# Performance work log

Measured on AMD Instinct MI355X. Metric: run time of the kernel, lower is better.

The kernel has to match this reference:

```python
import jax, jax.numpy as jnp
import numpy as np

NUM_BUCKETS = 32
MAX_DISTANCE = 128
NEG = -1000000.0


def t5_position_bucket(seq_len):
    # distances from the single query (at position seq_len-1) to keys 0..seq_len-1
    n = (seq_len - 1) - jnp.arange(seq_len)  # nonnegative, decreasing to 0
    max_exact = NUM_BUCKETS // 2
    is_small = n < max_exact
    large = max_exact + (
        jnp.log(jnp.maximum(n, 1).astype(jnp.float32) / max_exact)
        / np.log(MAX_DISTANCE / max_exact)
        * (NUM_BUCKETS - max_exact)
    ).astype(jnp.int32)
    large = jnp.minimum(large, NUM_BUCKETS - 1)
    return jnp.where(is_small, n, large).astype(jnp.float32)


def setup_inputs() -> dict:
    key = jax.random.key(0)
    ks = jax.random.split(key, 10)
    B, H, hd, T = 8, 16, 128, 2048  # head_dim = 1024//16 + 64 = 128; D = H*hd = 2048
    D = H * hd
    scale = 0.02
    return {
        "t": T,
        "content_t": jax.random.normal(ks[0], (B, D), jnp.float32),
        "time_mask": jax.random.randint(ks[1], (B, T + 1), 0, 2, jnp.int32),
        "cache": jax.random.normal(ks[2], (B, T, D), jnp.float32),
        "speakers": jax.random.randint(ks[3], (B,), 0, 2),
        "Wq": jax.random.normal(ks[4], (H, hd, hd), jnp.float32) * scale,
        "bq": jnp.zeros((H, hd), jnp.float32),
        "Wk": jax.random.normal(ks[5], (H, hd, hd), jnp.float32) * scale,
        "bk": jnp.zeros((H, hd), jnp.float32),
        "Wv": jax.random.normal(ks[6], (H, hd, hd), jnp.float32) * scale,
        "bv": jnp.zeros((H, hd), jnp.float32),
        "pos_param": jnp.asarray(0.02, jnp.float32),
    }


def reference(t, content_t, time_mask, cache, speakers, Wq, bq, Wk, bk, Wv, bv, pos_param):
    B, D = content_t.shape
    H, hd, _ = Wq.shape
    S = t + 1
    LOCAL_WINDOW = 256

    cnt = content_t.reshape(B, H, hd)                       # per-head query token
    cache_h = cache.reshape(B, t, H, hd)
    cache_full = jnp.concatenate([cache_h, cnt[:, None]], axis=1)  # (B, S, H, hd)

    q = jnp.einsum("bhd,hde->bhe", cnt, Wq) + bq            # (B, H, hd)
    k = jnp.einsum("bshd,hde->bshe", cache_full, Wk) + bk   # (B, S, H, hd)
    v = jnp.einsum("bshd,hde->bshe", cache_full, Wv) + bv

    scores = jnp.einsum("bhe,bshe->bhs", q, k) / (hd ** 0.5)  # (B, H, S)

    pos = t5_position_bucket(S)                             # (S,)
    scores = scores - pos_param * pos[None, None, :]

    # faithful masked_fill sequence: 1 -> 0, then every 0 -> -1e6
    tm = time_mask[:, :S].astype(scores.dtype)
    tm = jnp.where(tm == 1.0, 0.0, tm)
    tm = jnp.where(tm == 0.0, NEG, tm)
    scores = scores + tm[:, None, :]

    # local attention: mask everything before the last LOCAL_WINDOW positions
    if S > LOCAL_WINDOW:
        cutoff = S - LOCAL_WINDOW
        local = jnp.where(jnp.arange(S) < cutoff, NEG, 0.0).astype(scores.dtype)
        scores = scores + local[None, None, :]

    attn = jax.nn.softmax(scores, axis=-1)                  # (B, H, S)
    out = jnp.einsum("bhs,bshe->bhe", attn, v).reshape(B, D)
    return out + content_t
```

## Files before the change

### kernel.cpp

```cpp
#include <hip/hip_runtime.h>
#include <math.h>

#define WINDOW_MAX 256
#define NEG -1000000.0f

typedef __attribute__((address_space(1))) const float gfloat;
typedef __attribute__((address_space(3))) float lfloat;

__global__ __launch_bounds__(512, 2) void bca_fast(
    const float* __restrict__ content,
    const float* __restrict__ cache,
    const float* __restrict__ Wq,
    const float* __restrict__ bq,
    const float* __restrict__ Wk,
    const float* __restrict__ Wv,
    const float* __restrict__ bv,
    const float* __restrict__ pos_param_p,
    float* __restrict__ out,
    int B, int T, int D, int H, int S, int cutoff)
{
    constexpr int HD  = 128;
    constexpr int WIN = 256;

    __shared__ float xs[WIN * HD];
    __shared__ float qp[2][HD];
    __shared__ float kp[2][HD];
    __shared__ float kfull[HD];
    __shared__ float scp[2][WIN];
    __shared__ float sc[WIN];
    __shared__ float wp[16][HD];
    __shared__ float ws[HD];
    __shared__ float op[4][HD];
    __shared__ float red2[8];

    const int tid = threadIdx.x;
    const int h = blockIdx.x, b = blockIdx.y;
    const float* cnt_g = content + (size_t)b * D + h * HD;
    const float* cb    = cache + (size_t)b * T * D + h * HD;

    const float pos_param = pos_param_p[0];
    const int e128 = tid & 127;
    const int g4   = tid >> 7;
    const int d4   = tid & 31;
    const int sg   = tid >> 5;
    float creg = 0.f, bvreg = 0.f;
    if (tid < HD) { creg = cnt_g[tid]; bvreg = bv[h * HD + tid]; }

    float wvreg[32];

    if (tid < 256) {
        const int g2 = g4;
        float4 wk4[16];
        {
            const float* wkp = Wk + h * HD * HD + e128 * HD + g2 * 64;
            #pragma unroll
            for (int j = 0; j < 16; ++j) wk4[j] = *(const float4*)(wkp + j * 4);
        }
        const float* wqp = Wq + h * HD * HD + (g2 * 64) * HD + e128;
        const float* cg  = cnt_g + g2 * 64;
        float acc = (g2 == 0) ? bq[h * HD + e128] : 0.f;
        #pragma unroll
        for (int i = 0; i < 64; ++i)
            acc = fmaf(cg[i], wqp[i * HD], acc);
        qp[g2][e128] = acc;

        __syncthreads();

        float a2 = 0.f;
        #pragma unroll
        for (int j = 0; j < 16; ++j) {
            const float4 q0 = *(const float4*)&qp[0][g2 * 64 + j * 4];
            const float4 q1 = *(const float4*)&qp[1][g2 * 64 + j * 4];
            a2 = fmaf(wk4[j].x, q0.x + q1.x, a2);
            a2 = fmaf(wk4[j].y, q0.y + q1.y, a2);
            a2 = fmaf(wk4[j].z, q0.z + q1.z, a2);
            a2 = fmaf(wk4[j].w, q0.w + q1.w, a2);
        }
        kp[g2][e128] = a2;
    } else {
        const int sw   = (tid >> 6) - 4;
        const int lane = tid & 63;
        #pragma unroll
        for (int i = 0; i < 32; ++i) {
            const int w    = sw * 64 + i * 2;
            const int row  = w + (lane >> 5);
            const int f    = (lane & 31) ^ (row & 7);
            const int gpos = cutoff + row;
            const float* src = (gpos < T) ? (cb + (size_t)gpos * D + f * 4)
                                          : (cnt_g + f * 4);
            __builtin_amdgcn_global_load_lds((gfloat*)src, (lfloat*)&xs[w << 7],
                                             16, 0, 0);
        }
        __syncthreads();
    }
    __syncthreads();

    {
        const float* wvp = Wv + h * HD * HD + (g4 * 32) * HD + e128;
        #pragma unroll
        for (int i = 0; i < 32; ++i) wvreg[i] = wvp[i * HD];
    }

    if (tid < HD) kfull[tid] = kp[0][tid] + kp[1][tid];
    __syncthreads();

    {
        const int s = tid & 255, dh = tid >> 8;
        const int swz = s & 7;
        float acc = 0.f;
        #pragma unroll
        for (int j = 0; j < 16; ++j) {
            const int c = (dh * 16 + j) ^ swz;
            const float4 x  = *(const float4*)&xs[(s << 7) + (c << 2)];
            const float4 kf = *(const float4*)&kfull[dh * 64 + j * 4];
            acc = fmaf(x.x, kf.x, acc);
            acc = fmaf(x.y, kf.y, acc);
            acc = fmaf(x.z, kf.z, acc);
            acc = fmaf(x.w, kf.w, acc);
        }
        scp[dh][s] = acc;
    }
    __syncthreads();

    float p = 0.f;
    if (tid < WIN) {
        const float dot = scp[0][tid] + scp[1][tid];
        const int n = (WIN - 1) - tid;
        float posb;
        if (n < 16) {
            posb = (float)n;
        } else {
            const float lc = 2.0794415416798357f;
            int large = 16 + (int)((logf((float)n / 16.0f) / lc) * 16.0f);
            if (large > 31) large = 31;
            posb = (float)large;
        }
        const float score = (dot / 11.313708498984761f) - pos_param * posb + NEG;
        p = expf(score - NEG);
        sc[tid] = p;
    }
    float ssum = p;
    #pragma unroll
    for (int off = 32; off >= 1; off >>= 1) ssum += __shfl_xor(ssum, off);
    if ((tid & 63) == 0) red2[tid >> 6] = ssum;
    __syncthreads();

    {
        float4 wacc = make_float4(0.f, 0.f, 0.f, 0.f);
        #pragma unroll
        for (int ii = 0; ii < 4; ++ii) {
            const float4 ps = *(const float4*)&sc[sg * 16 + ii * 4];
            const float pw[4] = { ps.x, ps.y, ps.z, ps.w };
            #pragma unroll
            for (int k = 0; k < 4; ++k) {
                const int r = sg * 16 + ii * 4 + k;
                const int c = d4 ^ (r & 7);
                const float4 x = *(const float4*)&xs[(r << 7) + (c << 2)];
                wacc.x = fmaf(pw[k], x.x, wacc.x);
                wacc.y = fmaf(pw[k], x.y, wacc.y);
                wacc.z = fmaf(pw[k], x.z, wacc.z);
                wacc.w = fmaf(pw[k], x.w, wacc.w);
            }
        }
        *(float4*)&wp[sg][d4 << 2] = wacc;
    }
    __syncthreads();

    if (tid < HD) {
        float t = 0.f;
        #pragma unroll
        for (int s2 = 0; s2 < 16; ++s2) t += wp[s2][tid];
        ws[tid] = t;
    }
    __syncthreads();

    {
        float acc = 0.f;
        #pragma unroll
        for (int i = 0; i < 32; ++i)
            acc = fmaf(ws[g4 * 32 + i], wvreg[i], acc);
        op[g4][e128] = acc;
    }
    __syncthreads();

    if (tid < HD) {
        float SUM = red2[0];
        #pragma unroll
        for (int i = 1; i < 8; ++i) SUM += red2[i];
        const float r = (op[0][tid] + op[1][tid] + op[2][tid] + op[3][tid])
                        * (1.0f / SUM) + bvreg + creg;
        out[(size_t)b * D + h * HD + tid] = r;
    }
}

__global__ __launch_bounds__(256) void bca_generic(
    const float* __restrict__ content, const float* __restrict__ cache,
    const float* __restrict__ Wq, const float* __restrict__ bq,
    const float* __restrict__ Wk, const float* __restrict__ Wv,
    const float* __restrict__ bv, const float* __restrict__ pos_param_p,
    float* __restrict__ out,
    int B, int T, int D, int H, int S, int window, int cutoff)
{
    constexpr int HD = 128;
    constexpr int XP = HD + 1;
    const int bh = blockIdx.x;
    const int b = bh / H, h = bh % H;
    const int tid = threadIdx.x;

    __shared__ float xs[WINDOW_MAX * XP];
    __shared__ float cnt_s[HD];
    __shared__ float q_s[HD];
    __shared__ float qk_s[HD];
    __shared__ float sc_s[WINDOW_MAX];
    __shared__ float part_s[256];
    __shared__ float wsum_s[HD];
    __shared__ float red_s[4];

    const float* cnt_g = content + (size_t)b * D + (size_t)h * HD;
    if (tid < HD) cnt_s[tid] = cnt_g[tid];

    const int total4 = window * (HD / 4);
    for (int idx = tid; idx < total4; idx += blockDim.x) {
        const int w = idx >> 5, f = idx & 31;
        const int gpos = cutoff + w;
        const float* src = (gpos < T)
            ? (cache + (size_t)b * T * D + (size_t)gpos * D + (size_t)h * HD)
            : cnt_g;
        const float4 v4 = *(const float4*)(src + f * 4);
        float* dst = &xs[w * XP + f * 4];
        dst[0] = v4.x; dst[1] = v4.y; dst[2] = v4.z; dst[3] = v4.w;
    }
    __syncthreads();

    if (tid < HD) {
        const float* wq = Wq + (size_t)h * HD * HD;
        float acc = 0.f;
        #pragma unroll 8
        for (int d = 0; d < HD; ++d) acc = fmaf(cnt_s[d], wq[d * HD + tid], acc);
        q_s[tid] = acc + bq[h * HD + tid];
    }
    __syncthreads();

    if (tid < HD) {
        const float* wk = Wk + (size_t)h * HD * HD + (size_t)tid * HD;
        float acc = 0.f;
        #pragma unroll 8
        for (int e = 0; e < HD; e += 4) {
            const float4 w4 = *(const float4*)(wk + e);
            acc = fmaf(w4.x, q_s[e],     acc);
            acc = fmaf(w4.y, q_s[e + 1], acc);
            acc = fmaf(w4.z, q_s[e + 2], acc);
            acc = fmaf(w4.w, q_s[e + 3], acc);
        }
        qk_s[tid] = acc;
    }
    __syncthreads();

    const float pos_param = pos_param_p[0];
    float score = -INFINITY;
    if (tid < window) {
        float acc = 0.f;
        const float* xr = &xs[tid * XP];
        #pragma unroll 8
        for (int d = 0; d < HD; ++d) acc = fmaf(qk_s[d], xr[d], acc);
        const int gpos = cutoff + tid;
        const int n = (S - 1) - gpos;
        float posb;
        if (n < 16) posb = (float)n;
        else {
            const float lc = 2.0794415416798357f;
            int large = 16 + (int)((logf((float)n / 16.0f) / lc) * 16.0f);
            if (large > 31) large = 31;
            posb = (float)large;
        }
        score = (acc / 11.313708498984761f) - pos_param * posb + NEG;
    }

    float m = score;
    #pragma unroll
    for (int off = 32; off >= 1; off >>= 1) m = fmaxf(m, __shfl_xor(m, off));
    if ((tid & 63) == 0) red_s[tid >> 6] = m;
    __syncthreads();
    const int nw = blockDim.x >> 6;
    float M = red_s[0];
    for (int i = 1; i < nw; ++i) M = fmaxf(M, red_s[i]);

    float p = (tid < window) ? expf(score - M) : 0.f;
    float ssum = p;
    #pragma unroll
    for (int off = 32; off >= 1; off >>= 1) ssum += __shfl_xor(ssum, off);
    __syncthreads();
    if ((tid & 63) == 0) red_s[tid >> 6] = ssum;
    __syncthreads();
    float SUM = 0.f;
    for (int i = 0; i < nw; ++i) SUM += red_s[i];
    const float inv = 1.0f / SUM;
    if (tid < window) sc_s[tid] = p * inv;
    __syncthreads();

    {
        const int d = tid & (HD - 1), half = tid >> 7;
        const int s0 = half * (window >> 1), s1 = s0 + (window >> 1);
        float acc = 0.f;
        for (int s = s0; s < s1; ++s) acc = fmaf(sc_s[s], xs[s * XP + d], acc);
        part_s[tid] = acc;
    }
    __syncthreads();
    if (tid < HD) wsum_s[tid] = part_s[tid] + part_s[tid + HD];
    __syncthreads();

    {
        const int e = tid & (HD - 1), dh = tid >> 7;
        const float* wv = Wv + (size_t)h * HD * HD;
        float acc = 0.f;
        for (int d = dh * 64; d < dh * 64 + 64; ++d)
            acc = fmaf(wsum_s[d], wv[d * HD + e], acc);
        part_s[tid] = acc;
    }
    __syncthreads();
    if (tid < HD) {
        const float r = part_s[tid] + part_s[tid + HD]
                      + bv[h * HD + tid] + cnt_g[tid];
        out[(size_t)b * D + (size_t)h * HD + tid] = r;
    }
}

extern "C" void kernel_launch(void* const* d_in, const int* in_sizes, int n_in,
                              void* d_out, int out_size, void* d_ws, size_t ws_size,
                              hipStream_t stream) {
    const float* content = (const float*)d_in[1];
    const float* cache   = (const float*)d_in[3];
    const float* Wq      = (const float*)d_in[5];
    const float* bq      = (const float*)d_in[6];
    const float* Wk      = (const float*)d_in[7];
    const float* Wv      = (const float*)d_in[9];
    const float* bv      = (const float*)d_in[10];
    const float* posp    = (const float*)d_in[11];

    const int D  = in_sizes[6];
    const int B  = in_sizes[1] / D;
    const int hd = in_sizes[5] / D;
    const int H  = D / hd;
    const int T  = in_sizes[3] / (B * D);
    const int S  = T + 1;
    const int window = (S < WINDOW_MAX) ? S : WINDOW_MAX;
    const int cutoff = S - window;

    if (window == WINDOW_MAX && hd == 128) {
        dim3 grid(H, B), block(512);
        hipLaunchKernelGGL(bca_fast, grid, block, 0, stream,
                           content, cache, Wq, bq, Wk, Wv, bv, posp,
                           (float*)d_out, B, T, D, H, S, cutoff);
    } else {
        dim3 grid(B * H), block(256);
        hipLaunchKernelGGL(bca_generic, grid, block, 0, stream,
                           content, cache, Wq, bq, Wk, Wv, bv, posp,
                           (float*)d_out, B, T, D, H, S, window, cutoff);
    }
}
```

Baseline: 14.40 us.

## Split attention window across two blocks per head with a combine kernel

The attention kernel now launches two blocks per (batch, head), each handling half of the 256-row local window. Each block writes its unnormalized weighted V output and its partial softmax denominator to a workspace. A second small kernel sums the two halves, normalizes, and adds the bias and residual. The aim is to double the block count so more CUs are busy and each block stages half the cache rows. In exchange, the Q/K/V weight loads and projections are repeated in both blocks, and there is an extra kernel launch plus a workspace round trip.

```diff
diff --git a/kernel.cpp b/kernel.cpp
--- a/kernel.cpp
+++ b/kernel.cpp
@@ -7,34 +7,35 @@
 typedef __attribute__((address_space(1))) const float gfloat;
 typedef __attribute__((address_space(3))) float lfloat;
 
-__global__ __launch_bounds__(512, 2) void bca_fast(
+#define WS_STRIDE 132
+
+__global__ __launch_bounds__(512, 2) void bca_half(
     const float* __restrict__ content,
     const float* __restrict__ cache,
     const float* __restrict__ Wq,
     const float* __restrict__ bq,
     const float* __restrict__ Wk,
     const float* __restrict__ Wv,
-    const float* __restrict__ bv,
     const float* __restrict__ pos_param_p,
-    float* __restrict__ out,
+    float* __restrict__ wsp,
     int B, int T, int D, int H, int S, int cutoff)
 {
-    constexpr int HD  = 128;
-    constexpr int WIN = 256;
-
-    __shared__ float xs[WIN * HD];
+    constexpr int HD = 128;
+    constexpr int NR = 128;
+
+    __shared__ float xs[NR * HD];
     __shared__ float qp[2][HD];
     __shared__ float kp[2][HD];
     __shared__ float kfull[HD];
-    __shared__ float scp[2][WIN];
-    __shared__ float sc[WIN];
+    __shared__ float scp[4][NR];
+    __shared__ float sc[NR];
     __shared__ float wp[16][HD];
-    __shared__ float ws[HD];
+    __shared__ float wsum_s[HD];
     __shared__ float op[4][HD];
-    __shared__ float red2[8];
-
-    const int tid = threadIdx.x;
-    const int h = blockIdx.x, b = blockIdx.y;
+    __shared__ float red2[2];
+
+    const int tid  = threadIdx.x;
+    const int h    = blockIdx.x, b = blockIdx.y, half = blockIdx.z;
     const float* cnt_g = content + (size_t)b * D + h * HD;
     const float* cb    = cache + (size_t)b * T * D + h * HD;
 
@@ -43,8 +44,7 @@
     const int g4   = tid >> 7;
     const int d4   = tid & 31;
     const int sg   = tid >> 5;
-    float creg = 0.f, bvreg = 0.f;
-    if (tid < HD) { creg = cnt_g[tid]; bvreg = bv[h * HD + tid]; }
+    const int base = half * NR;
 
     float wvreg[32];
 
@@ -81,11 +81,11 @@
         const int sw   = (tid >> 6) - 4;
         const int lane = tid & 63;
         #pragma unroll
-        for (int i = 0; i < 32; ++i) {
-            const int w    = sw * 64 + i * 2;
+        for (int i = 0; i < 16; ++i) {
+            const int w    = sw * 32 + i * 2;
             const int row  = w + (lane >> 5);
             const int f    = (lane & 31) ^ (row & 7);
-            const int gpos = cutoff + row;
+            const int gpos = cutoff + base + row;
             const float* src = (gpos < T) ? (cb + (size_t)gpos * D + f * 4)
                                           : (cnt_g + f * 4);
             __builtin_amdgcn_global_load_lds((gfloat*)src, (lfloat*)&xs[w << 7],
@@ -105,27 +105,27 @@
     __syncthreads();
 
     {
-        const int s = tid & 255, dh = tid >> 8;
+        const int s = tid & 127, dq = tid >> 7;
         const int swz = s & 7;
         float acc = 0.f;
         #pragma unroll
-        for (int j = 0; j < 16; ++j) {
-            const int c = (dh * 16 + j) ^ swz;
+        for (int j = 0; j < 8; ++j) {
+            const int c = (dq * 8 + j) ^ swz;
             const float4 x  = *(const float4*)&xs[(s << 7) + (c << 2)];
-            const float4 kf = *(const float4*)&kfull[dh * 64 + j * 4];
+            const float4 kf = *(const float4*)&kfull[dq * 32 + j * 4];
             acc = fmaf(x.x, kf.x, acc);
             acc = fmaf(x.y, kf.y, acc);
             acc = fmaf(x.z, kf.z, acc);
             acc = fmaf(x.w, kf.w, acc);
         }
-        scp[dh][s] = acc;
+        scp[dq][s] = acc;
     }
     __syncthreads();
 
     float p = 0.f;
-    if (tid < WIN) {
-        const float dot = scp[0][tid] + scp[1][tid];
-        const int n = (WIN - 1) - tid;
+    if (tid < NR) {
+        const float dot = scp[0][tid] + scp[1][tid] + scp[2][tid] + scp[3][tid];
+        const int n = (WINDOW_MAX - 1) - (base + tid);
         float posb;
         if (n < 16) {
             posb = (float)n;
@@ -142,18 +142,18 @@
     float ssum = p;
     #pragma unroll
     for (int off = 32; off >= 1; off >>= 1) ssum += __shfl_xor(ssum, off);
-    if ((tid & 63) == 0) red2[tid >> 6] = ssum;
+    if (tid < NR && (tid & 63) == 0) red2[tid >> 6] = ssum;
     __syncthreads();
 
     {
         float4 wacc = make_float4(0.f, 0.f, 0.f, 0.f);
         #pragma unroll
-        for (int ii = 0; ii < 4; ++ii) {
-            const float4 ps = *(const float4*)&sc[sg * 16 + ii * 4];
+        for (int ii = 0; ii < 2; ++ii) {
+            const float4 ps = *(const float4*)&sc[sg * 8 + ii * 4];
             const float pw[4] = { ps.x, ps.y, ps.z, ps.w };
             #pragma unroll
             for (int k = 0; k < 4; ++k) {
-                const int r = sg * 16 + ii * 4 + k;
+                const int r = sg * 8 + ii * 4 + k;
                 const int c = d4 ^ (r & 7);
                 const float4 x = *(const float4*)&xs[(r << 7) + (c << 2)];
                 wacc.x = fmaf(pw[k], x.x, wacc.x);
@@ -170,7 +170,7 @@
         float t = 0.f;
         #pragma unroll
         for (int s2 = 0; s2 < 16; ++s2) t += wp[s2][tid];
-        ws[tid] = t;
+        wsum_s[tid] = t;
     }
     __syncthreads();
 
@@ -178,19 +178,34 @@
         float acc = 0.f;
         #pragma unroll
         for (int i = 0; i < 32; ++i)
-            acc = fmaf(ws[g4 * 32 + i], wvreg[i], acc);
+            acc = fmaf(wsum_s[g4 * 32 + i], wvreg[i], acc);
         op[g4][e128] = acc;
     }
     __syncthreads();
 
-    if (tid < HD) {
-        float SUM = red2[0];
-        #pragma unroll
-        for (int i = 1; i < 8; ++i) SUM += red2[i];
-        const float r = (op[0][tid] + op[1][tid] + op[2][tid] + op[3][tid])
-                        * (1.0f / SUM) + bvreg + creg;
-        out[(size_t)b * D + h * HD + tid] = r;
-    }
+    float* slot = wsp + ((size_t)(b * H + h) * 2 + half) * WS_STRIDE;
+    if (tid < HD)
+        slot[tid] = op[0][tid] + op[1][tid] + op[2][tid] + op[3][tid];
+    if (tid == 0)
+        slot[HD] = red2[0] + red2[1];
+}
+
+__global__ __launch_bounds__(256) void bca_combine(
+    const float* __restrict__ wsp,
+    const float* __restrict__ content,
+    const float* __restrict__ bv,
+    float* __restrict__ out,
+    int H, int total)
+{
+    const int idx = blockIdx.x * 256 + threadIdx.x;
+    if (idx >= total) return;
+    const int bh = idx >> 7, e = idx & 127;
+    const float* s0 = wsp + ((size_t)bh * 2 + 0) * WS_STRIDE;
+    const float* s1 = wsp + ((size_t)bh * 2 + 1) * WS_STRIDE;
+    const float SUM = s0[128] + s1[128];
+    const float r = (s0[e] + s1[e]) * (1.0f / SUM)
+                  + bv[(bh % H) * 128 + e] + content[idx];
+    out[idx] = r;
 }
 
 __global__ __launch_bounds__(256) void bca_generic(
@@ -347,10 +362,15 @@
     const int cutoff = S - window;
 
     if (window == WINDOW_MAX && hd == 128) {
-        dim3 grid(H, B), block(512);
-        hipLaunchKernelGGL(bca_fast, grid, block, 0, stream,
-                           content, cache, Wq, bq, Wk, Wv, bv, posp,
-                           (float*)d_out, B, T, D, H, S, cutoff);
+        float* wsp = (float*)d_ws;
+        dim3 grid1(H, B, 2), block1(512);
+        hipLaunchKernelGGL(bca_half, grid1, block1, 0, stream,
+                           content, cache, Wq, bq, Wk, Wv, posp,
+                           wsp, B, T, D, H, S, cutoff);
+        const int total = B * H * 128;
+        dim3 grid2((total + 255) / 256), block2(256);
+        hipLaunchKernelGGL(bca_combine, grid2, block2, 0, stream,
+                           wsp, content, bv, (float*)d_out, H, total);
     } else {
         dim3 grid(B * H), block(256);
         hipLaunchKernelGGL(bca_generic, grid, block, 0, stream,
```

Result: slower. 15.02 us (+4.3%).
